# Kernel optimization log

Hardware: AMD Instinct MI355X
Metric: run time of the kernel (lower is better)

The kernel has to match this reference:

```python
import jax, jax.numpy as jnp
import numpy as np

B, H, W, C = 64, 32, 32, 384          # batch, spatial resolution, channels
NH, WS = 12, 7                        # num_heads, window_size
HD = C // NH                          # head_dim = key_dim (attn_ratio=1)
MLP_H = 4 * C                         # mlp_ratio=4
SCALE = HD ** -0.5
EPS = 1e-5


def _bias_idxs():
    # replicate Attention.__init__ relative-position index construction
    pts = [(i, j) for i in range(WS) for j in range(WS)]
    offs, idxs = {}, []
    for p1 in pts:
        for p2 in pts:
            o = (abs(p1[0] - p2[0]), abs(p1[1] - p2[1]))
            if o not in offs:
                offs[o] = len(offs)
            idxs.append(offs[o])
    return np.array(idxs, dtype=np.int32).reshape(WS * WS, WS * WS), len(offs)


def setup_inputs() -> dict:
    key = jax.random.key(0)
    ks = jax.random.split(key, 8)
    idxs, n_off = _bias_idxs()
    s = lambda k, shape: jax.random.normal(k, shape, jnp.float32) * 0.02
    return {
        'x': jax.random.normal(ks[0], (B, H * W, C), jnp.float32),
        'ln1_g': jnp.ones((C,), jnp.float32), 'ln1_b': jnp.zeros((C,), jnp.float32),
        'qkv_w': s(ks[1], (C, 3 * C)), 'qkv_b': jnp.zeros((3 * C,), jnp.float32),
        'proj_w': s(ks[2], (C, C)), 'proj_b': jnp.zeros((C,), jnp.float32),
        'attn_biases': s(ks[3], (NH, n_off)),
        'conv_w': s(ks[4], (C, 1, 3, 3)),
        'bn_g': jnp.ones((C,), jnp.float32), 'bn_b': jnp.zeros((C,), jnp.float32),
        'bn_m': jnp.zeros((C,), jnp.float32), 'bn_v': jnp.ones((C,), jnp.float32),
        'ln2_g': jnp.ones((C,), jnp.float32), 'ln2_b': jnp.zeros((C,), jnp.float32),
        'fc1_w': s(ks[5], (C, MLP_H)), 'fc1_b': jnp.zeros((MLP_H,), jnp.float32),
        'fc2_w': s(ks[6], (MLP_H, C)), 'fc2_b': jnp.zeros((C,), jnp.float32),
        'bias_idxs': jnp.asarray(idxs),
    }


def _ln(x, g, b):
    m = x.mean(-1, keepdims=True)
    v = ((x - m) ** 2).mean(-1, keepdims=True)
    return (x - m) * jax.lax.rsqrt(v + EPS) * g + b


def _block(x, ln1_g, ln1_b, qkv_w, qkv_b, proj_w, proj_b, attn_biases,
           conv_w, bn_g, bn_b, bn_m, bn_v, ln2_g, ln2_b,
           fc1_w, fc1_b, fc2_w, fc2_b, bias_idxs):
    Bb, L, Cc = x.shape
    res = x
    # ---- window partition with padding ----
    xi = x.reshape(Bb, H, W, Cc)
    pad_b = (WS - H % WS) % WS
    pad_r = (WS - W % WS) % WS
    xi = jnp.pad(xi, ((0, 0), (0, pad_b), (0, pad_r), (0, 0)))
    pH, pW = H + pad_b, W + pad_r
    nHw, nWw = pH // WS, pW // WS
    xw = (xi.reshape(Bb, nHw, WS, nWw, WS, Cc)
            .transpose(0, 1, 3, 2, 4, 5)
            .reshape(Bb * nHw * nWw, WS * WS, Cc))
    # ---- windowed attention with gathered relative-position bias ----
    Bw, N, _ = xw.shape
    xn = _ln(xw, ln1_g, ln1_b)
    qkv = (xn @ qkv_w + qkv_b).reshape(Bw, N, NH, 3 * HD)
    q, k, v = jnp.split(qkv, 3, axis=-1)              # each [Bw, N, NH, HD]
    ab = attn_biases[:, bias_idxs]                     # gather -> [NH, N, N]
    attn = jnp.einsum('bnhd,bmhd->bhnm', q, k) * SCALE + ab
    attn = jax.nn.softmax(attn, axis=-1)
    aw = jnp.einsum('bhnm,bmhd->bnhd', attn, v).reshape(Bw, N, Cc)
    aw = aw @ proj_w + proj_b
    # ---- window merge / unpad ----
    xi = (aw.reshape(Bb, nHw, nWw, WS, WS, Cc)
            .transpose(0, 1, 3, 2, 4, 5)
            .reshape(Bb, pH, pW, Cc))[:, :H, :W]
    x = res + xi.reshape(Bb, L, Cc)
    # ---- depthwise 3x3 conv + BN (eval semantics), NCHW ----
    xc = x.transpose(0, 2, 1).reshape(Bb, Cc, H, W)
    xc = jax.lax.conv_general_dilated(xc, conv_w, (1, 1), ((1, 1), (1, 1)),
                                      feature_group_count=Cc)
    xc = ((xc - bn_m[:, None, None]) * jax.lax.rsqrt(bn_v[:, None, None] + 1e-5)
          * bn_g[:, None, None] + bn_b[:, None, None])
    x = xc.reshape(Bb, Cc, L).transpose(0, 2, 1)
    # ---- MLP (LayerNorm -> fc1 -> GELU -> fc2), residual ----
    h = jax.nn.gelu(_ln(x, ln2_g, ln2_b) @ fc1_w + fc1_b, approximate=False)
    return x + (h @ fc2_w + fc2_b)


def reference(x, ln1_g, ln1_b, qkv_w, qkv_b, proj_w, proj_b, attn_biases,
              conv_w, bn_g, bn_b, bn_m, bn_v, ln2_g, ln2_b,
              fc1_w, fc1_b, fc2_w, fc2_b, bias_idxs):
    return _block(x, ln1_g, ln1_b, qkv_w, qkv_b, proj_w, proj_b, attn_biases,
                  conv_w, bn_g, bn_b, bn_m, bn_v, ln2_g, ln2_b,
                  fc1_w, fc1_b, fc2_w, fc2_b, bias_idxs)
```

## Files before the change

### kernel.cpp

```cpp
#include <hip/hip_runtime.h>
#include <hip/hip_bf16.h>
#include <math.h>

#define NHEAD 12
#define CDIM 384
#define QKVC 1152
#define MLPH 1536
#define SCALE 0.17677669529663687f

typedef __attribute__((ext_vector_type(8))) short short8;
typedef __attribute__((ext_vector_type(4))) float f32x4;

static __device__ __forceinline__ unsigned short f2bf(float f) {
  union { __hip_bfloat16 b; unsigned short u; } c;
  c.b = __float2bfloat16(f);
  return c.u;
}

__global__ void ln_kernel(const float* __restrict__ X, const float* __restrict__ g,
                          const float* __restrict__ b, __hip_bfloat16* __restrict__ Y, int T) {
  int wid = (blockIdx.x * blockDim.x + threadIdx.x) >> 6;
  int lane = threadIdx.x & 63;
  if (wid >= T) return;
  const float* x = X + (size_t)wid * CDIM;
  float vals[6];
  float s = 0.f;
#pragma unroll
  for (int i = 0; i < 6; i++) { vals[i] = x[lane + i * 64]; s += vals[i]; }
#pragma unroll
  for (int o = 32; o > 0; o >>= 1) s += __shfl_xor(s, o);
  float m = s * (1.f / 384.f);
  float vs = 0.f;
#pragma unroll
  for (int i = 0; i < 6; i++) { float d = vals[i] - m; vs += d * d; }
#pragma unroll
  for (int o = 32; o > 0; o >>= 1) vs += __shfl_xor(vs, o);
  float rs = rsqrtf(vs * (1.f / 384.f) + 1e-5f);
  __hip_bfloat16* y = Y + (size_t)wid * CDIM;
#pragma unroll
  for (int i = 0; i < 6; i++) {
    int c = lane + i * 64;
    y[c] = __float2bfloat16((vals[i] - m) * rs * g[c] + b[c]);
  }
}

__global__ void pad_qkv_kernel(const float* __restrict__ lb, const float* __restrict__ Wq,
                               const float* __restrict__ bq, __hip_bfloat16* __restrict__ outp) {
  int j = blockIdx.x * blockDim.x + threadIdx.x;
  if (j >= QKVC) return;
  float s = bq[j];
  for (int c = 0; c < CDIM; c++) s += lb[c] * Wq[(size_t)c * QKVC + j];
  outp[j] = __float2bfloat16(s);
}

__global__ void expand_bias(const float* __restrict__ biases, const int* __restrict__ bidx,
                            float* __restrict__ Bexp, int n_off) {
  int h = blockIdx.x;
  for (int e = threadIdx.x; e < 4096; e += 256) {
    int n = e >> 6, m = e & 63;
    float v;
    if (m >= 49) v = -1e30f;
    else if (n >= 49) v = 0.f;
    else v = biases[h * n_off + bidx[n * 49 + m]];
    Bexp[h * 4096 + e] = v;
  }
}

__global__ void wt_convert(const float* __restrict__ W, __hip_bfloat16* __restrict__ Wt,
                           int K, int N) {
  __shared__ float t[32][33];
  int n0 = blockIdx.x * 32, k0 = blockIdx.y * 32;
  int tx = threadIdx.x, ty = threadIdx.y;
#pragma unroll
  for (int i = 0; i < 4; i++) t[ty + i * 8][tx] = W[(size_t)(k0 + ty + i * 8) * N + n0 + tx];
  __syncthreads();
#pragma unroll
  for (int i = 0; i < 4; i++)
    Wt[(size_t)(n0 + ty + i * 8) * K + k0 + tx] = __float2bfloat16(t[tx][ty + i * 8]);
}

template <int GELU, int HAS_RES, int OUT_BF16>
__global__ __launch_bounds__(256) void gemm_mfma(
    const __hip_bfloat16* __restrict__ A, const __hip_bfloat16* __restrict__ Bt,
    const float* __restrict__ bias, const float* __restrict__ res,
    void* __restrict__ Cout, int M, int N, int K) {
  __shared__ unsigned short Al[128][72];
  __shared__ unsigned short Bl[64][72];
  int tid = threadIdx.x;
  int m0 = blockIdx.y * 128, n0 = blockIdx.x * 64;
  int wave = tid >> 6, lane = tid & 63;
  int wm = (wave >> 1) * 64, wn = (wave & 1) * 32;
  int l15 = lane & 15, l4 = lane >> 4;

  int am = tid >> 1, ak = (tid & 1) * 32;
  int bn = tid >> 2, bk = (tid & 3) * 16;
  const __hip_bfloat16* Ag = A + (size_t)(m0 + am) * K + ak;
  const __hip_bfloat16* Bg = Bt + (size_t)(n0 + bn) * K + bk;

  f32x4 acc[4][2] = {};

  for (int kt = 0; kt < K; kt += 64) {
    uint4 av0 = *(const uint4*)(Ag + kt);
    uint4 av1 = *(const uint4*)(Ag + kt + 8);
    uint4 av2 = *(const uint4*)(Ag + kt + 16);
    uint4 av3 = *(const uint4*)(Ag + kt + 24);
    uint4 bv0 = *(const uint4*)(Bg + kt);
    uint4 bv1 = *(const uint4*)(Bg + kt + 8);
    __syncthreads();
    *(uint4*)&Al[am][ak]      = av0;
    *(uint4*)&Al[am][ak + 8]  = av1;
    *(uint4*)&Al[am][ak + 16] = av2;
    *(uint4*)&Al[am][ak + 24] = av3;
    *(uint4*)&Bl[bn][bk]      = bv0;
    *(uint4*)&Bl[bn][bk + 8]  = bv1;
    __syncthreads();
#pragma unroll
    for (int kk = 0; kk < 64; kk += 32) {
      short8 af[4], bfr[2];
#pragma unroll
      for (int i = 0; i < 4; i++)
        af[i] = *(const short8*)&Al[wm + i * 16 + l15][kk + l4 * 8];
#pragma unroll
      for (int j = 0; j < 2; j++)
        bfr[j] = *(const short8*)&Bl[wn + j * 16 + l15][kk + l4 * 8];
#pragma unroll
      for (int i = 0; i < 4; i++)
#pragma unroll
        for (int j = 0; j < 2; j++)
          acc[i][j] = __builtin_amdgcn_mfma_f32_16x16x32_bf16(af[i], bfr[j], acc[i][j], 0, 0, 0);
    }
  }

#pragma unroll
  for (int i = 0; i < 4; i++) {
#pragma unroll
    for (int j = 0; j < 2; j++) {
      int n = n0 + wn + j * 16 + l15;
      float bv = bias[n];
#pragma unroll
      for (int r = 0; r < 4; r++) {
        int m = m0 + wm + i * 16 + l4 * 4 + r;
        float c = acc[i][j][r] + bv;
        if (GELU) c = 0.5f * c * (1.f + erff(c * 0.70710678118654752f));
        if (HAS_RES) c += res[(size_t)m * N + n];
        if (OUT_BF16)
          ((__hip_bfloat16*)Cout)[(size_t)m * N + n] = __float2bfloat16(c);
        else
          ((float*)Cout)[(size_t)m * N + n] = c;
      }
    }
  }
}

__global__ __launch_bounds__(64) void attn_mfma(
    const __hip_bfloat16* __restrict__ qkv, const __hip_bfloat16* __restrict__ qkv_pad,
    const float* __restrict__ Bexp, __hip_bfloat16* __restrict__ aw) {
  int h = blockIdx.x % NHEAD;
  int w = blockIdx.x / NHEAD;
  int b = w / 25, wi = w % 25;
  int wh = wi / 5, wv = wi % 5;

  __shared__ unsigned short Q[64][40];
  __shared__ unsigned short K[64][40];
  __shared__ unsigned short Vt[32][72];
  __shared__ unsigned short P[64][72];

  int lane = threadIdx.x;
  int l15 = lane & 15, l4 = lane >> 4;

  {
    int t = lane;
    uint4 z = {0, 0, 0, 0};
    uint4 qv[4], kv[4];
    union { uint4 u[4]; unsigned short s[32]; } vu;
    bool use = t < 49;
    const unsigned short* src = (const unsigned short*)qkv_pad + h * 96;
    if (use) {
      int hh = wh * 7 + t / 7, ww = wv * 7 + t % 7;
      if (hh < 32 && ww < 32)
        src = (const unsigned short*)qkv + (size_t)(b * 1024 + hh * 32 + ww) * QKVC + h * 96;
    }
#pragma unroll
    for (int c = 0; c < 4; c++) {
      qv[c]   = use ? *(const uint4*)(src + c * 8)      : z;
      kv[c]   = use ? *(const uint4*)(src + 32 + c * 8) : z;
      vu.u[c] = use ? *(const uint4*)(src + 64 + c * 8) : z;
    }
#pragma unroll
    for (int c = 0; c < 4; c++) {
      *(uint4*)&Q[t][c * 8] = qv[c];
      *(uint4*)&K[t][c * 8] = kv[c];
    }
#pragma unroll
    for (int d = 0; d < 32; d++) Vt[d][t] = vu.s[d];
  }
  __syncthreads();

  f32x4 acc[4][4] = {};
  {
    short8 aq[4], bk[4];
#pragma unroll
    for (int i = 0; i < 4; i++) aq[i] = *(const short8*)&Q[i * 16 + l15][l4 * 8];
#pragma unroll
    for (int j = 0; j < 4; j++) bk[j] = *(const short8*)&K[j * 16 + l15][l4 * 8];
#pragma unroll
    for (int i = 0; i < 4; i++)
#pragma unroll
      for (int j = 0; j < 4; j++)
        acc[i][j] = __builtin_amdgcn_mfma_f32_16x16x32_bf16(aq[i], bk[j], acc[i][j], 0, 0, 0);
  }

  const float* Bh = Bexp + h * 4096;
  float rinv_[4][4];
#pragma unroll
  for (int i = 0; i < 4; i++) {
    float s[4][4];
#pragma unroll
    for (int j = 0; j < 4; j++)
#pragma unroll
      for (int r = 0; r < 4; r++) {
        int n = i * 16 + l4 * 4 + r, m = j * 16 + l15;
        s[j][r] = acc[i][j][r] * SCALE + Bh[n * 64 + m];
      }
#pragma unroll
    for (int r = 0; r < 4; r++) {
      float mx = fmaxf(fmaxf(s[0][r], s[1][r]), fmaxf(s[2][r], s[3][r]));
#pragma unroll
      for (int o = 1; o < 16; o <<= 1) mx = fmaxf(mx, __shfl_xor(mx, o));
      float p[4], sm = 0.f;
#pragma unroll
      for (int j = 0; j < 4; j++) { p[j] = __expf(s[j][r] - mx); sm += p[j]; }
#pragma unroll
      for (int o = 1; o < 16; o <<= 1) sm += __shfl_xor(sm, o);
      rinv_[i][r] = 1.f / sm;
      int n = i * 16 + l4 * 4 + r;
#pragma unroll
      for (int j = 0; j < 4; j++) P[n][j * 16 + l15] = f2bf(p[j]);
    }
  }
  __syncthreads();

  f32x4 o[4][2] = {};
#pragma unroll
  for (int ks = 0; ks < 2; ks++) {
    short8 pa[4], vb[2];
#pragma unroll
    for (int i = 0; i < 4; i++) pa[i] = *(const short8*)&P[i * 16 + l15][ks * 32 + l4 * 8];
#pragma unroll
    for (int j = 0; j < 2; j++) vb[j] = *(const short8*)&Vt[j * 16 + l15][ks * 32 + l4 * 8];
#pragma unroll
    for (int i = 0; i < 4; i++)
#pragma unroll
      for (int j = 0; j < 2; j++)
        o[i][j] = __builtin_amdgcn_mfma_f32_16x16x32_bf16(pa[i], vb[j], o[i][j], 0, 0, 0);
  }

#pragma unroll
  for (int i = 0; i < 4; i++)
#pragma unroll
    for (int r = 0; r < 4; r++) {
      int n = i * 16 + l4 * 4 + r;
      if (n < 49) {
        int hh = wh * 7 + n / 7, ww = wv * 7 + n % 7;
        if (hh < 32 && ww < 32) {
          __hip_bfloat16* dst = aw + (size_t)(b * 1024 + hh * 32 + ww) * CDIM + h * 32;
          float ri = rinv_[i][r];
#pragma unroll
          for (int j = 0; j < 2; j++)
            dst[j * 16 + l15] = __float2bfloat16(o[i][j][r] * ri);
        }
      }
    }
}

__global__ __launch_bounds__(384) void conv_bn_ln_kernel(
    const float* __restrict__ X, const float* __restrict__ W9,
    const float* __restrict__ g, const float* __restrict__ bb,
    const float* __restrict__ mm, const float* __restrict__ vv,
    const float* __restrict__ lg, const float* __restrict__ lb,
    float* __restrict__ X2, __hip_bfloat16* __restrict__ XN) {
  int nwg = gridDim.x;
  int id = blockIdx.x;
  int nid = (id & 7) * (nwg >> 3) + (id >> 3);
  int yh = nid & 1;
  int x = (nid >> 1) & 31;
  int b = nid >> 6;
  int c = threadIdx.x;

  float w[9];
#pragma unroll
  for (int i = 0; i < 9; i++) w[i] = W9[c * 9 + i];
  float bnsc = rsqrtf(vv[c] + 1e-5f) * g[c];
  float bnsh = bb[c] - mm[c] * bnsc;
  float lgc = lg[c], lbc = lb[c];

  bool xm = x > 0, xp = x < 31;
  const float* colbase = X + ((size_t)(b * 1024 + x)) * CDIM + c;

  __shared__ float part[2][6][2];
  int wv = threadIdx.x >> 6, ln = threadIdx.x & 63;

  float w0[3], w1[3], w2[3];
  int y0 = yh * 16;
  if (y0 == 0) {
    w0[0] = w0[1] = w0[2] = 0.f;
  } else {
    const float* p = colbase + (size_t)(y0 - 1) * 32 * CDIM;
    w0[0] = xm ? p[-CDIM] : 0.f; w0[1] = p[0]; w0[2] = xp ? p[CDIM] : 0.f;
  }
  {
    const float* p = colbase + (size_t)y0 * 32 * CDIM;
    w1[0] = xm ? p[-CDIM] : 0.f; w1[1] = p[0]; w1[2] = xp ? p[CDIM] : 0.f;
  }

  for (int y = y0; y < y0 + 16; y++) {
    if (y + 1 < 32) {
      const float* p = colbase + (size_t)(y + 1) * 32 * CDIM;
      w2[0] = xm ? p[-CDIM] : 0.f; w2[1] = p[0]; w2[2] = xp ? p[CDIM] : 0.f;
    } else {
      w2[0] = w2[1] = w2[2] = 0.f;
    }
    float acc = w0[0] * w[0] + w0[1] * w[1] + w0[2] * w[2]
              + w1[0] * w[3] + w1[1] * w[4] + w1[2] * w[5]
              + w2[0] * w[6] + w2[1] * w[7] + w2[2] * w[8];
    float r = acc * bnsc + bnsh;
    size_t tok = (size_t)(b * 1024 + y * 32 + x);
    X2[tok * CDIM + c] = r;

    float s1 = r, s2 = r * r;
#pragma unroll
    for (int o = 32; o > 0; o >>= 1) { s1 += __shfl_xor(s1, o); s2 += __shfl_xor(s2, o); }
    int pb = y & 1;
    if (ln == 0) { part[pb][wv][0] = s1; part[pb][wv][1] = s2; }
    __syncthreads();
    float ts1 = 0.f, ts2 = 0.f;
#pragma unroll
    for (int i = 0; i < 6; i++) { ts1 += part[pb][i][0]; ts2 += part[pb][i][1]; }
    float mean = ts1 * (1.f / 384.f);
    float var = ts2 * (1.f / 384.f) - mean * mean;
    float rstd = rsqrtf(var + 1e-5f);
    XN[tok * CDIM + c] = __float2bfloat16((r - mean) * rstd * lgc + lbc);

    w0[0] = w1[0]; w0[1] = w1[1]; w0[2] = w1[2];
    w1[0] = w2[0]; w1[1] = w2[1]; w1[2] = w2[2];
  }
}

extern "C" void kernel_launch(void* const* d_in, const int* in_sizes, int n_in,
                              void* d_out, int out_size, void* d_ws, size_t ws_size,
                              hipStream_t stream) {
  const float* x      = (const float*)d_in[0];
  const float* ln1_g  = (const float*)d_in[1];
  const float* ln1_b  = (const float*)d_in[2];
  const float* qkv_w  = (const float*)d_in[3];
  const float* qkv_b  = (const float*)d_in[4];
  const float* proj_w = (const float*)d_in[5];
  const float* proj_b = (const float*)d_in[6];
  const float* att_b  = (const float*)d_in[7];
  const float* conv_w = (const float*)d_in[8];
  const float* bn_g   = (const float*)d_in[9];
  const float* bn_b   = (const float*)d_in[10];
  const float* bn_m   = (const float*)d_in[11];
  const float* bn_v   = (const float*)d_in[12];
  const float* ln2_g  = (const float*)d_in[13];
  const float* ln2_b  = (const float*)d_in[14];
  const float* fc1_w  = (const float*)d_in[15];
  const float* fc1_b  = (const float*)d_in[16];
  const float* fc2_w  = (const float*)d_in[17];
  const float* fc2_b  = (const float*)d_in[18];
  const int* bias_idxs = (const int*)d_in[19];
  int n_off = in_sizes[7] / NHEAD;
  float* out = (float*)d_out;

  char* ws = (char*)d_ws;
  size_t off = 0;
  __hip_bfloat16* qkv_pad = (__hip_bfloat16*)(ws + off); off += QKVC * 2;
  off = (off + 255) & ~(size_t)255;
  float* Bexp = (float*)(ws + off); off += (size_t)NHEAD * 4096 * 4;
  __hip_bfloat16* wqkvT = (__hip_bfloat16*)(ws + off); off += (size_t)QKVC * CDIM * 2;
  __hip_bfloat16* wprojT = (__hip_bfloat16*)(ws + off); off += (size_t)CDIM * CDIM * 2;
  __hip_bfloat16* wfc1T = (__hip_bfloat16*)(ws + off); off += (size_t)MLPH * CDIM * 2;
  __hip_bfloat16* wfc2T = (__hip_bfloat16*)(ws + off); off += (size_t)CDIM * MLPH * 2;
  size_t HDR = (off + 255) & ~(size_t)255;

  const size_t PER_TOK = 9984;
  int Bc = 64;
  while (Bc > 1 && HDR + (size_t)Bc * 1024 * PER_TOK > ws_size) Bc >>= 1;
  size_t Tc = (size_t)Bc * 1024;

  off = HDR;
  __hip_bfloat16* xn = (__hip_bfloat16*)(ws + off); off += Tc * CDIM * 2;
  __hip_bfloat16* qkv = (__hip_bfloat16*)(ws + off); off += Tc * QKVC * 2;
  __hip_bfloat16* awb = (__hip_bfloat16*)(ws + off); off += Tc * CDIM * 2;
  float* x1 = (float*)(ws + off); off += Tc * CDIM * 4;
  float* x2 = (float*)(ws + off); off += Tc * CDIM * 4;
  __hip_bfloat16* hb = (__hip_bfloat16*)(ws + off); off += Tc * MLPH * 2;

  pad_qkv_kernel<<<dim3(5), dim3(256), 0, stream>>>(ln1_b, qkv_w, qkv_b, qkv_pad);
  expand_bias<<<dim3(NHEAD), dim3(256), 0, stream>>>(att_b, bias_idxs, Bexp, n_off);
  wt_convert<<<dim3(QKVC / 32, CDIM / 32), dim3(32, 8), 0, stream>>>(qkv_w, wqkvT, CDIM, QKVC);
  wt_convert<<<dim3(CDIM / 32, CDIM / 32), dim3(32, 8), 0, stream>>>(proj_w, wprojT, CDIM, CDIM);
  wt_convert<<<dim3(MLPH / 32, CDIM / 32), dim3(32, 8), 0, stream>>>(fc1_w, wfc1T, CDIM, MLPH);
  wt_convert<<<dim3(CDIM / 32, MLPH / 32), dim3(32, 8), 0, stream>>>(fc2_w, wfc2T, MLPH, CDIM);

  for (int b0 = 0; b0 < 64; b0 += Bc) {
    const float* xa = x + (size_t)b0 * 1024 * CDIM;
    float* outa = out + (size_t)b0 * 1024 * CDIM;
    int M = (int)Tc;

    ln_kernel<<<dim3(M / 4), dim3(256), 0, stream>>>(xa, ln1_g, ln1_b, xn, M);
    gemm_mfma<0, 0, 1><<<dim3(QKVC / 64, M / 128), dim3(256), 0, stream>>>(
        xn, wqkvT, qkv_b, nullptr, qkv, M, QKVC, CDIM);
    attn_mfma<<<dim3(Bc * 25 * NHEAD), dim3(64), 0, stream>>>(qkv, qkv_pad, Bexp, awb);
    gemm_mfma<0, 1, 0><<<dim3(CDIM / 64, M / 128), dim3(256), 0, stream>>>(
        awb, wprojT, proj_b, xa, x1, M, CDIM, CDIM);
    conv_bn_ln_kernel<<<dim3(Bc * 64), dim3(384), 0, stream>>>(
        x1, conv_w, bn_g, bn_b, bn_m, bn_v, ln2_g, ln2_b, x2, xn);
    gemm_mfma<1, 0, 1><<<dim3(MLPH / 64, M / 128), dim3(256), 0, stream>>>(
        xn, wfc1T, fc1_b, nullptr, hb, M, MLPH, CDIM);
    gemm_mfma<0, 1, 0><<<dim3(CDIM / 64, M / 128), dim3(256), 0, stream>>>(
        hb, wfc2T, fc2_b, x2, outa, M, CDIM, MLPH);
  }
}
```

Measured before the change: 861.6 us.

## Enlarge GEMM tile to 128x128 and remap blocks with XCD-aware swizzle

Each GEMM block now computes a 128x128 output tile instead of 128x64, with each wave holding a 4x4 grid of MFMA accumulators, which doubles operand reuse per LDS load. The grid becomes 1D and block indices are permuted in strides of eight so that consecutive tiles land on the same XCD, which should improve L2 sharing. The trade-off is fewer blocks, which may underfill the CUs on the N=384 GEMMs, plus higher register use.

```diff
diff --git a/kernel.cpp b/kernel.cpp
--- a/kernel.cpp
+++ b/kernel.cpp
@@ -83,50 +83,51 @@
 __global__ __launch_bounds__(256) void gemm_mfma(
     const __hip_bfloat16* __restrict__ A, const __hip_bfloat16* __restrict__ Bt,
     const float* __restrict__ bias, const float* __restrict__ res,
-    void* __restrict__ Cout, int M, int N, int K) {
+    void* __restrict__ Cout, int M, int N, int K, int gx) {
   __shared__ unsigned short Al[128][72];
-  __shared__ unsigned short Bl[64][72];
+  __shared__ unsigned short Bl[128][72];
+  int T = gridDim.x;
+  int f = blockIdx.x;
+  int t = (f & 7) * (T >> 3) + (f >> 3);
+  int n0 = (t % gx) * 128, m0 = (t / gx) * 128;
   int tid = threadIdx.x;
-  int m0 = blockIdx.y * 128, n0 = blockIdx.x * 64;
   int wave = tid >> 6, lane = tid & 63;
-  int wm = (wave >> 1) * 64, wn = (wave & 1) * 32;
+  int wm = (wave >> 1) * 64, wn = (wave & 1) * 64;
   int l15 = lane & 15, l4 = lane >> 4;
 
-  int am = tid >> 1, ak = (tid & 1) * 32;
-  int bn = tid >> 2, bk = (tid & 3) * 16;
-  const __hip_bfloat16* Ag = A + (size_t)(m0 + am) * K + ak;
-  const __hip_bfloat16* Bg = Bt + (size_t)(n0 + bn) * K + bk;
-
-  f32x4 acc[4][2] = {};
+  int row = tid >> 1, cg = (tid & 1) * 32;
+  const __hip_bfloat16* Ag = A + (size_t)(m0 + row) * K + cg;
+  const __hip_bfloat16* Bg = Bt + (size_t)(n0 + row) * K + cg;
+
+  f32x4 acc[4][4] = {};
 
   for (int kt = 0; kt < K; kt += 64) {
-    uint4 av0 = *(const uint4*)(Ag + kt);
-    uint4 av1 = *(const uint4*)(Ag + kt + 8);
-    uint4 av2 = *(const uint4*)(Ag + kt + 16);
-    uint4 av3 = *(const uint4*)(Ag + kt + 24);
-    uint4 bv0 = *(const uint4*)(Bg + kt);
-    uint4 bv1 = *(const uint4*)(Bg + kt + 8);
+    uint4 av[4], bv[4];
+#pragma unroll
+    for (int i = 0; i < 4; i++) {
+      av[i] = *(const uint4*)(Ag + kt + i * 8);
+      bv[i] = *(const uint4*)(Bg + kt + i * 8);
+    }
     __syncthreads();
-    *(uint4*)&Al[am][ak]      = av0;
-    *(uint4*)&Al[am][ak + 8]  = av1;
-    *(uint4*)&Al[am][ak + 16] = av2;
-    *(uint4*)&Al[am][ak + 24] = av3;
-    *(uint4*)&Bl[bn][bk]      = bv0;
-    *(uint4*)&Bl[bn][bk + 8]  = bv1;
+#pragma unroll
+    for (int i = 0; i < 4; i++) {
+      *(uint4*)&Al[row][cg + i * 8] = av[i];
+      *(uint4*)&Bl[row][cg + i * 8] = bv[i];
+    }
     __syncthreads();
 #pragma unroll
     for (int kk = 0; kk < 64; kk += 32) {
-      short8 af[4], bfr[2];
+      short8 af[4], bfr[4];
 #pragma unroll
       for (int i = 0; i < 4; i++)
         af[i] = *(const short8*)&Al[wm + i * 16 + l15][kk + l4 * 8];
 #pragma unroll
-      for (int j = 0; j < 2; j++)
+      for (int j = 0; j < 4; j++)
         bfr[j] = *(const short8*)&Bl[wn + j * 16 + l15][kk + l4 * 8];
 #pragma unroll
       for (int i = 0; i < 4; i++)
 #pragma unroll
-        for (int j = 0; j < 2; j++)
+        for (int j = 0; j < 4; j++)
           acc[i][j] = __builtin_amdgcn_mfma_f32_16x16x32_bf16(af[i], bfr[j], acc[i][j], 0, 0, 0);
     }
   }
@@ -134,7 +135,7 @@
 #pragma unroll
   for (int i = 0; i < 4; i++) {
 #pragma unroll
-    for (int j = 0; j < 2; j++) {
+    for (int j = 0; j < 4; j++) {
       int n = n0 + wn + j * 16 + l15;
       float bv = bias[n];
 #pragma unroll
@@ -407,18 +408,19 @@
     const float* xa = x + (size_t)b0 * 1024 * CDIM;
     float* outa = out + (size_t)b0 * 1024 * CDIM;
     int M = (int)Tc;
+    int mt = M / 128;
 
     ln_kernel<<<dim3(M / 4), dim3(256), 0, stream>>>(xa, ln1_g, ln1_b, xn, M);
-    gemm_mfma<0, 0, 1><<<dim3(QKVC / 64, M / 128), dim3(256), 0, stream>>>(
-        xn, wqkvT, qkv_b, nullptr, qkv, M, QKVC, CDIM);
+    gemm_mfma<0, 0, 1><<<dim3((QKVC / 128) * mt), dim3(256), 0, stream>>>(
+        xn, wqkvT, qkv_b, nullptr, qkv, M, QKVC, CDIM, QKVC / 128);
     attn_mfma<<<dim3(Bc * 25 * NHEAD), dim3(64), 0, stream>>>(qkv, qkv_pad, Bexp, awb);
-    gemm_mfma<0, 1, 0><<<dim3(CDIM / 64, M / 128), dim3(256), 0, stream>>>(
-        awb, wprojT, proj_b, xa, x1, M, CDIM, CDIM);
+    gemm_mfma<0, 1, 0><<<dim3((CDIM / 128) * mt), dim3(256), 0, stream>>>(
+        awb, wprojT, proj_b, xa, x1, M, CDIM, CDIM, CDIM / 128);
     conv_bn_ln_kernel<<<dim3(Bc * 64), dim3(384), 0, stream>>>(
         x1, conv_w, bn_g, bn_b, bn_m, bn_v, ln2_g, ln2_b, x2, xn);
-    gemm_mfma<1, 0, 1><<<dim3(MLPH / 64, M / 128), dim3(256), 0, stream>>>(
-        xn, wfc1T, fc1_b, nullptr, hb, M, MLPH, CDIM);
-    gemm_mfma<0, 1, 0><<<dim3(CDIM / 64, M / 128), dim3(256), 0, stream>>>(
-        hb, wfc2T, fc2_b, x2, outa, M, CDIM, MLPH);
-  }
-}
+    gemm_mfma<1, 0, 1><<<dim3((MLPH / 128) * mt), dim3(256), 0, stream>>>(
+        xn, wfc1T, fc1_b, nullptr, hb, M, MLPH, CDIM, MLPH / 128);
+    gemm_mfma<0, 1, 0><<<dim3((CDIM / 128) * mt), dim3(256), 0, stream>>>(
+        hb, wfc2T, fc2_b, x2, outa, M, CDIM, MLPH, CDIM / 128);
+  }
+}
```

Measured after the change: 1.601 ms. 85.8% more time.

## Fuse fc1+GELU+fc2 MLP into one kernel keeping hidden activations in LDS

Applied to the files above, without the earlier changes.

Replaces the two MLP GEMM launches with a single kernel. Each block loads a 64-row tile of normalized input, computes 128-column chunks of fc1 with GELU into shared memory, and immediately accumulates them into the fc2 output. This removes the large bf16 hidden-activation buffer write and read in global memory and shrinks per-token workspace. In exchange, weight fragments are read directly from global memory per block without LDS staging, and there are more in-loop barriers.

```diff
diff --git a/kernel.cpp b/kernel.cpp
--- a/kernel.cpp
+++ b/kernel.cpp
@@ -150,6 +150,89 @@
       }
     }
   }
+}
+
+__global__ __launch_bounds__(512) void mlp_fused(
+    const __hip_bfloat16* __restrict__ XN, const __hip_bfloat16* __restrict__ W1T,
+    const float* __restrict__ B1, const __hip_bfloat16* __restrict__ W2T,
+    const float* __restrict__ B2, const float* __restrict__ X2,
+    float* __restrict__ OUT) {
+  __shared__ unsigned short XNl[64][392];
+  __shared__ unsigned short Hl[64][136];
+  int tid = threadIdx.x;
+  int m0 = blockIdx.x * 64;
+  int wave = tid >> 6, lane = tid & 63;
+  int wm = (wave >> 2) * 32;
+  int wn = wave & 3;
+  int l15 = lane & 15, l4 = lane >> 4;
+
+  {
+    int r = tid >> 3, seg = (tid & 7) * 48;
+    const unsigned short* src = (const unsigned short*)XN + (size_t)(m0 + r) * 384 + seg;
+#pragma unroll
+    for (int i = 0; i < 6; i++)
+      *(uint4*)&XNl[r][seg + i * 8] = *(const uint4*)(src + i * 8);
+  }
+
+  f32x4 acc[2][6] = {};
+  __syncthreads();
+
+  for (int ks = 0; ks < 12; ks++) {
+    f32x4 hacc[2][2] = {};
+    const unsigned short* w1b =
+        (const unsigned short*)W1T + ((size_t)ks * 128 + wn * 32) * 384 + l4 * 8;
+#pragma unroll
+    for (int kk = 0; kk < 384; kk += 32) {
+      short8 bf0 = *(const short8*)(w1b + (size_t)l15 * 384 + kk);
+      short8 bf1 = *(const short8*)(w1b + (size_t)(16 + l15) * 384 + kk);
+      short8 af0 = *(const short8*)&XNl[wm + l15][kk + l4 * 8];
+      short8 af1 = *(const short8*)&XNl[wm + 16 + l15][kk + l4 * 8];
+      hacc[0][0] = __builtin_amdgcn_mfma_f32_16x16x32_bf16(af0, bf0, hacc[0][0], 0, 0, 0);
+      hacc[0][1] = __builtin_amdgcn_mfma_f32_16x16x32_bf16(af0, bf1, hacc[0][1], 0, 0, 0);
+      hacc[1][0] = __builtin_amdgcn_mfma_f32_16x16x32_bf16(af1, bf0, hacc[1][0], 0, 0, 0);
+      hacc[1][1] = __builtin_amdgcn_mfma_f32_16x16x32_bf16(af1, bf1, hacc[1][1], 0, 0, 0);
+    }
+    float b10 = B1[ks * 128 + wn * 32 + l15];
+    float b11 = B1[ks * 128 + wn * 32 + 16 + l15];
+    __syncthreads();
+#pragma unroll
+    for (int i = 0; i < 2; i++)
+#pragma unroll
+      for (int j = 0; j < 2; j++) {
+        float bv = j ? b11 : b10;
+#pragma unroll
+        for (int r = 0; r < 4; r++) {
+          float c = hacc[i][j][r] + bv;
+          c = 0.5f * c * (1.f + erff(c * 0.70710678118654752f));
+          Hl[wm + i * 16 + l4 * 4 + r][wn * 32 + j * 16 + l15] = f2bf(c);
+        }
+      }
+    __syncthreads();
+    const unsigned short* w2b = (const unsigned short*)W2T + (size_t)ks * 128 + l4 * 8;
+#pragma unroll
+    for (int kk = 0; kk < 128; kk += 32) {
+      short8 af20 = *(const short8*)&Hl[wm + l15][kk + l4 * 8];
+      short8 af21 = *(const short8*)&Hl[wm + 16 + l15][kk + l4 * 8];
+#pragma unroll
+      for (int j = 0; j < 6; j++) {
+        short8 bf2 = *(const short8*)(w2b + (size_t)(wn * 96 + j * 16 + l15) * 1536 + kk);
+        acc[0][j] = __builtin_amdgcn_mfma_f32_16x16x32_bf16(af20, bf2, acc[0][j], 0, 0, 0);
+        acc[1][j] = __builtin_amdgcn_mfma_f32_16x16x32_bf16(af21, bf2, acc[1][j], 0, 0, 0);
+      }
+    }
+  }
+#pragma unroll
+  for (int i = 0; i < 2; i++)
+#pragma unroll
+    for (int j = 0; j < 6; j++) {
+      int n = wn * 96 + j * 16 + l15;
+      float bv = B2[n];
+#pragma unroll
+      for (int r = 0; r < 4; r++) {
+        int m = m0 + wm + i * 16 + l4 * 4 + r;
+        OUT[(size_t)m * 384 + n] = acc[i][j][r] + bv + X2[(size_t)m * 384 + n];
+      }
+    }
 }
 
 __global__ __launch_bounds__(64) void attn_mfma(
@@ -383,7 +466,7 @@
   __hip_bfloat16* wfc2T = (__hip_bfloat16*)(ws + off); off += (size_t)CDIM * MLPH * 2;
   size_t HDR = (off + 255) & ~(size_t)255;
 
-  const size_t PER_TOK = 9984;
+  const size_t PER_TOK = 6912;
   int Bc = 64;
   while (Bc > 1 && HDR + (size_t)Bc * 1024 * PER_TOK > ws_size) Bc >>= 1;
   size_t Tc = (size_t)Bc * 1024;
@@ -394,7 +477,6 @@
   __hip_bfloat16* awb = (__hip_bfloat16*)(ws + off); off += Tc * CDIM * 2;
   float* x1 = (float*)(ws + off); off += Tc * CDIM * 4;
   float* x2 = (float*)(ws + off); off += Tc * CDIM * 4;
-  __hip_bfloat16* hb = (__hip_bfloat16*)(ws + off); off += Tc * MLPH * 2;
 
   pad_qkv_kernel<<<dim3(5), dim3(256), 0, stream>>>(ln1_b, qkv_w, qkv_b, qkv_pad);
   expand_bias<<<dim3(NHEAD), dim3(256), 0, stream>>>(att_b, bias_idxs, Bexp, n_off);
@@ -416,9 +498,7 @@
         awb, wprojT, proj_b, xa, x1, M, CDIM, CDIM);
     conv_bn_ln_kernel<<<dim3(Bc * 64), dim3(384), 0, stream>>>(
         x1, conv_w, bn_g, bn_b, bn_m, bn_v, ln2_g, ln2_b, x2, xn);
-    gemm_mfma<1, 0, 1><<<dim3(MLPH / 64, M / 128), dim3(256), 0, stream>>>(
-        xn, wfc1T, fc1_b, nullptr, hb, M, MLPH, CDIM);
-    gemm_mfma<0, 1, 0><<<dim3(CDIM / 64, M / 128), dim3(256), 0, stream>>>(
-        hb, wfc2T, fc2_b, x2, outa, M, CDIM, MLPH);
-  }
-}
+    mlp_fused<<<dim3(M / 64), dim3(512), 0, stream>>>(
+        xn, wfc1T, fc1_b, wfc2T, fc2_b, x2, outa);
+  }
+}
```

Result: slower. 1.062 ms (+23.3%).
